# Performance work log

Hardware: AMD Instinct MI355X
Metric: run time of the kernel (lower is better)

The kernel has to match this reference:

```python
import jax, jax.numpy as jnp
import numpy as np

B, LQ, S, D, H = 8, 1024, 256, 1024, 16
HD = D // H
LN_EPS = 1e-5


def layer_norm(x, g, b):
    m = jnp.mean(x, axis=-1, keepdims=True)
    v = jnp.mean((x - m) ** 2, axis=-1, keepdims=True)
    return (x - m) / jnp.sqrt(v + LN_EPS) * g + b


def setup_inputs() -> dict:
    key = jax.random.key(0)
    ks = jax.random.split(key, 12)
    sc = 0.02
    p = lambda k, shp: jax.random.normal(k, shp, dtype=jnp.float32) * sc
    return {
        "memory": jax.random.normal(ks[0], (B, LQ, D // 2), dtype=jnp.float32),
        "gaze_features": jax.random.normal(ks[1], (B, LQ, D // 2), dtype=jnp.float32),
        "text_features": jax.random.normal(ks[2], (B, S, D), dtype=jnp.float32),
        "w_in": p(ks[3], (3 * D, D)),  # packed q,k,v in_proj (torch MHA layout)
        "b_in": jnp.zeros((3 * D,), jnp.float32),
        "w_o": p(ks[4], (D, D)),
        "b_o": jnp.zeros((D,), jnp.float32),
        "w1": p(ks[5], (D, D)),
        "b1": jnp.zeros((D,), jnp.float32),
        "w2": p(ks[6], (D, D)),
        "b2": jnp.zeros((D,), jnp.float32),
        "g1": jnp.ones((D,), jnp.float32),
        "be1": jnp.zeros((D,), jnp.float32),
        "g2": jnp.ones((D,), jnp.float32),
        "be2": jnp.zeros((D,), jnp.float32),
    }


def reference(memory, gaze_features, text_features, w_in, b_in, w_o, b_o,
              w1, b1, w2, b2, g1, be1, g2, be2):
    combined = jnp.concatenate([memory, gaze_features], axis=-1)  # [B, LQ, D]
    wq, wk, wv = w_in[:D], w_in[D:2 * D], w_in[2 * D:]
    bq, bk, bv = b_in[:D], b_in[D:2 * D], b_in[2 * D:]

    q = (combined @ wq.T + bq).reshape(B, LQ, H, HD)
    k = (text_features @ wk.T + bk).reshape(B, S, H, HD)
    v = (text_features @ wv.T + bv).reshape(B, S, H, HD)

    scores = jnp.einsum("bqhd,bkhd->bhqk", q, k) / jnp.sqrt(jnp.float32(HD))
    attn_w = jax.nn.softmax(scores, axis=-1)
    ctx = jnp.einsum("bhqk,bkhd->bqhd", attn_w, v).reshape(B, LQ, D)
    attn_output = ctx @ w_o.T + b_o  # [B, LQ, D]

    # dual FFN branches share linear1/linear2 (as in the source); dropout = eval identity
    ffn = jax.nn.relu(attn_output @ w1.T + b1) @ w2.T + b2
    refpoint_embed = layer_norm(ffn, g1, be1)
    tgt = layer_norm(ffn, g2, be2)

    # vectorized box decode (replaces the per-element Python loop)
    s = jax.nn.sigmoid(attn_output[..., :4])
    xc, yc, w, h = s[..., 0], s[..., 1], s[..., 2], s[..., 3]
    init_box_proposal = jnp.stack(
        [xc - w / 2, yc - h / 2, xc + w / 2, yc + h / 2], axis=-1)  # [B, LQ, 4]

    return refpoint_embed, tgt, init_box_proposal
```

## Files before the change

### kernel.cpp

```cpp
#include <hip/hip_runtime.h>


typedef unsigned short u16;
typedef unsigned int u32;
typedef __bf16 bf16x8 __attribute__((ext_vector_type(8)));
typedef float f32x4 __attribute__((ext_vector_type(4)));
typedef u16 u16x4 __attribute__((ext_vector_type(4)));

struct CvtArgs { const void* in[15]; };

__device__ __forceinline__ u16 f2bf(float f) {
  u32 u = __builtin_bit_cast(u32, f);
  u += 0x7fffu + ((u >> 16) & 1u);
  return (u16)(u >> 16);
}
__device__ __forceinline__ float bf2f(u16 h) {
  u32 u = ((u32)h) << 16;
  return __builtin_bit_cast(float, u);
}

struct WsPtrs {
  u16 *c_mem, *c_gaze, *c_text, *c_win, *c_bin, *c_wo, *c_bo, *c_w1, *c_b1,
      *c_w2, *c_b2, *c_g1, *c_be1, *c_g2, *c_be2;
  u16 *q, *k, *v, *ctx, *woT, *wf, *bfb, *h1, *ffnb;
};
__device__ __forceinline__ WsPtrs wsp(u16* C) {
  WsPtrs w;
  w.c_mem = C;                 w.c_gaze = C + 4194304;   w.c_text = C + 8388608;
  w.c_win = C + 10485760;      w.c_bin = C + 13631488;   w.c_wo = C + 13634560;
  w.c_bo = C + 14683136;       w.c_w1 = C + 14684160;    w.c_b1 = C + 15732736;
  w.c_w2 = C + 15733760;       w.c_b2 = C + 16782336;    w.c_g1 = C + 16783360;
  w.c_be1 = C + 16784384;      w.c_g2 = C + 16785408;    w.c_be2 = C + 16786432;
  u16* B2 = C + 16787488;
  w.q = B2;                    w.k = B2 + 8388608;       w.v = B2 + 10485760;
  w.ctx = B2 + 12582912;
  w.woT = B2 + 20971520;
  w.wf  = B2 + 22020096;
  w.bfb = B2 + 23068672;
  w.h1  = B2 + 29360128;
  w.ffnb = B2;
  return w;
}

__device__ __forceinline__ void cvt_chunk(bool f32in, u16* dst,
                                          const void* const* srcs, u32 c8) {
  const u32 cum[16] = {0u, 4194304u, 8388608u, 10485760u, 13631488u, 13634560u,
                       14683136u, 14684160u, 15732736u, 15733760u, 16782336u,
                       16783360u, 16784384u, 16785408u, 16786432u, 16787456u};
  u32 base = c8 * 8u;
  int idx = 0;
#pragma unroll
  for (int i = 1; i < 15; ++i) if (base >= cum[i]) idx = i;
  u32 off = base - cum[idx];
  if (f32in) {
    const float* s = (const float*)srcs[idx] + off;
    float4 a = ((const float4*)s)[0];
    float4 b = ((const float4*)s)[1];
    u16 t[8] = {f2bf(a.x), f2bf(a.y), f2bf(a.z), f2bf(a.w),
                f2bf(b.x), f2bf(b.y), f2bf(b.z), f2bf(b.w)};
    *(uint4*)(dst + base) = *(const uint4*)t;
  } else {
    *(uint4*)(dst + base) = *(const uint4*)((const u16*)srcs[idx] + off);
  }
}

__global__ __launch_bounds__(256) void cvt_tr(CvtArgs a, u16* ws) {
  __shared__ u16 tile[128 * 136];
  const bool f32in = (((const u32*)a.in[11])[0] == 0x3F800000u);
  const int bid = blockIdx.x, tid = threadIdx.x;
  if (bid < 64) {
    WsPtrs w = wsp(ws);
    int tr = bid >> 3, tc = bid & 7;
#pragma unroll
    for (int p = 0; p < 8; ++p) {
      int t = p * 16 + (tid >> 4);
      int j8 = (tid & 15) * 8;
      u16 tmp[8];
      if (f32in) {
        const float* s = (const float*)a.in[5] + (size_t)(tr * 128 + t) * 1024 + tc * 128 + j8;
        float4 x = ((const float4*)s)[0], y = ((const float4*)s)[1];
        tmp[0]=f2bf(x.x); tmp[1]=f2bf(x.y); tmp[2]=f2bf(x.z); tmp[3]=f2bf(x.w);
        tmp[4]=f2bf(y.x); tmp[5]=f2bf(y.y); tmp[6]=f2bf(y.z); tmp[7]=f2bf(y.w);
      } else {
        *(uint4*)tmp = *(const uint4*)((const u16*)a.in[5] + (size_t)(tr * 128 + t) * 1024 + tc * 128 + j8);
      }
      *(uint4*)&tile[t * 136 + j8] = *(const uint4*)tmp;
    }
    __syncthreads();
#pragma unroll
    for (int p = 0; p < 8; ++p) {
      int j = p * 16 + (tid >> 4);
      int t8 = (tid & 15) * 8;
      u16 tmp[8];
#pragma unroll
      for (int i = 0; i < 8; ++i) tmp[i] = tile[(t8 + i) * 136 + j];
      *(uint4*)(w.woT + (size_t)(tc * 128 + j) * 1024 + tr * 128 + t8) = *(const uint4*)tmp;
    }
  } else {
    u32 c8 = (u32)(bid - 64) * 256u + tid;
    if (c8 < 2098432u) cvt_chunk(f32in, ws, a.in, c8);
  }
}

template <int TN>
__device__ __forceinline__ void gemm_core(
    u16* sA, u16* sB,
    const u16* A0, const u16* A1, int Ksplit, int lda0, int lda1,
    const u16* W, const u16* bias, void* out, int N, int K,
    int mode, int lg, int m0, int n0)
{
  constexpr int JN = TN >> 5;
  constexpr int BCPT = TN >> 5;
  const int tid = threadIdx.x;
  const int wave = tid >> 6, lane = tid & 63;
  const int quad = lane >> 4, l16 = lane & 15;
  const int wm = wave >> 1, wn = wave & 1;

  f32x4 acc[4][JN];
#pragma unroll
  for (int i = 0; i < 4; ++i)
#pragma unroll
    for (int j = 0; j < JN; ++j) acc[i][j] = (f32x4){0.f, 0.f, 0.f, 0.f};

  for (int k0 = 0; k0 < K; k0 += 64) {
#pragma unroll
    for (int qi = 0; qi < 4; ++qi) {
      int p = (wave * 4 + qi) * 64 + lane;
      int row = p >> 3;
      int c = (p & 7) ^ (row & 7);
      int gk = k0 + (c << 3);
      const u16* srcA = (gk < Ksplit) ? (A0 + (size_t)(m0 + row) * lda0 + gk)
                                      : (A1 + (size_t)(m0 + row) * lda1 + (gk - Ksplit));
      __builtin_amdgcn_global_load_lds(
          (const __attribute__((address_space(1))) void*)srcA,
          (__attribute__((address_space(3))) void*)&sA[(size_t)(wave * 4 + qi) * 512],
          16, 0, 0);
    }
#pragma unroll
    for (int qi = 0; qi < BCPT; ++qi) {
      int p = (wave * BCPT + qi) * 64 + lane;
      int row = p >> 3;
      int c = (p & 7) ^ (row & 7);
      int gk = k0 + (c << 3);
      const u16* srcB = W + (size_t)(n0 + row) * K + gk;
      __builtin_amdgcn_global_load_lds(
          (const __attribute__((address_space(1))) void*)srcB,
          (__attribute__((address_space(3))) void*)&sB[(size_t)(wave * BCPT + qi) * 512],
          16, 0, 0);
    }
    __syncthreads();
#pragma unroll
    for (int ks = 0; ks < 2; ++ks) {
      const int ch = (ks << 2) + quad;
      bf16x8 af[4], bw[JN];
#pragma unroll
      for (int i = 0; i < 4; ++i) {
        int row = wm * 64 + i * 16 + l16;
        af[i] = *(const bf16x8*)&sA[(row << 6) + ((ch ^ (row & 7)) << 3)];
      }
#pragma unroll
      for (int j = 0; j < JN; ++j) {
        int row = wn * (TN >> 1) + j * 16 + l16;
        bw[j] = *(const bf16x8*)&sB[(row << 6) + ((ch ^ (row & 7)) << 3)];
      }
#pragma unroll
      for (int i = 0; i < 4; ++i)
#pragma unroll
        for (int j = 0; j < JN; ++j)
          acc[i][j] = __builtin_amdgcn_mfma_f32_16x16x32_bf16(af[i], bw[j], acc[i][j], 0, 0, 0);
    }
    __syncthreads();
  }

#pragma unroll
  for (int i = 0; i < 4; ++i) {
#pragma unroll
    for (int j = 0; j < JN; ++j) {
      int n = n0 + wn * (TN >> 1) + j * 16 + l16;
      float bv = bias ? bf2f(bias[n]) : 0.f;
#pragma unroll
      for (int rr = 0; rr < 4; ++rr) {
        int m = m0 + wm * 64 + i * 16 + quad * 4 + rr;
        float val = acc[i][j][rr] + bv;
        if (mode == 1) val = fmaxf(val, 0.f);
        if (mode <= 1) {
          ((u16*)out)[(size_t)m * N + n] = f2bf(val);
        } else if (mode == 3) {
          int b = m >> lg, l = m & ((1 << lg) - 1);
          int h = n >> 6, d = n & 63;
          ((u16*)out)[((size_t)((b * 16 + h)) << (lg + 6)) + (l << 6) + d] = f2bf(val);
        } else {
          int b = m >> lg, s = m & ((1 << lg) - 1);
          int h = n >> 6, d = n & 63;
          ((u16*)out)[((size_t)(((b * 16 + h) << 6) + d) << lg) + s] = f2bf(val);
        }
      }
    }
  }
}

__device__ __forceinline__ int xswz(int u, int n8) {
  return (u & 7) * n8 + (u >> 3);
}

__global__ __launch_bounds__(256, 4) void qkvwf(u16* ws) {
  __shared__ __align__(16) u16 lds[16384];
  WsPtrs w = wsp(ws);
  const int bid = blockIdx.x, tid = threadIdx.x;
  if (bid < 512) {
    int u = xswz(bid, 64);
    gemm_core<128>(lds, lds + 8192, w.c_mem, w.c_gaze, 512, 512, 512,
                   w.c_win, w.c_bin, w.q, 1024, 1024, 3, 10,
                   (u >> 3) * 128, (u & 7) * 128);
  } else if (bid < 640) {
    int u = xswz(bid - 512, 16);
    gemm_core<128>(lds, lds + 8192, w.c_text, w.c_text, 1024, 1024, 1024,
                   w.c_win + 1048576, w.c_bin + 1024, w.k, 1024, 1024, 3, 8,
                   (u >> 3) * 128, (u & 7) * 128);
  } else if (bid < 768) {
    int u = xswz(bid - 640, 16);
    gemm_core<128>(lds, lds + 8192, w.c_text, w.c_text, 1024, 1024, 1024,
                   w.c_win + 2097152, w.c_bin + 2048, w.v, 1024, 1024, 4, 8,
                   (u >> 3) * 128, (u & 7) * 128);
  } else if (bid < 832) {
    int u = xswz(bid - 768, 8);
    gemm_core<128>(lds, lds + 8192, w.c_w1, w.c_w1, 1024, 1024, 1024,
                   w.woT, nullptr, w.wf, 1024, 1024, 0, 0,
                   (u >> 3) * 128, (u & 7) * 128);
  } else {
    int i = (bid - 832) * 256 + tid;
    const u16* w1row = w.c_w1 + (size_t)i * 1024;
    float acc = bf2f(w.c_b1[i]);
    for (int kk = 0; kk < 1024; kk += 8) {
      bf16x8 wv = *(const bf16x8*)(w1row + kk);
      bf16x8 bv = *(const bf16x8*)(w.c_bo + kk);
#pragma unroll
      for (int j = 0; j < 8; ++j) acc += (float)wv[j] * (float)bv[j];
    }
    w.bfb[i] = f2bf(acc);
  }
}

__global__ __launch_bounds__(256) void attn_kernel(u16* ws) {
  __shared__ u16 sV[64 * 256];
  __shared__ u16 sKP[256 * 64];
  WsPtrs w = wsp(ws);
  const int tid = threadIdx.x;
  const int wave = tid >> 6, lane = tid & 63;
  const int quad = lane >> 4, l16 = lane & 15;
  const int su = xswz(blockIdx.x, 256);
  const int qb = su & 15, bh = su >> 4;

  {
    int rr = tid >> 3, c8 = (tid & 7) << 3;
    const u16* kb = w.k + (size_t)bh * 16384;
#pragma unroll
    for (int p = 0; p < 8; ++p) {
      int row = p * 32 + rr;
      uint4 val = *(const uint4*)(kb + row * 64 + c8);
      *(uint4*)&sKP[(row << 6) + ((((c8 >> 3) ^ (row & 7))) << 3)] = val;
    }
    int r2 = tid >> 5, c8b = (tid & 31) << 3;
    const u16* vb = w.v + (size_t)bh * 16384;
#pragma unroll
    for (int p = 0; p < 8; ++p) {
      int row = p * 8 + r2;
      uint4 val = *(const uint4*)(vb + (row << 8) + c8b);
      *(uint4*)&sV[(row << 8) + ((((c8b >> 3) ^ (row & 7))) << 3)] = val;
    }
  }
  bf16x8 aq[2];
  {
    const u16* qrow = w.q + ((size_t)bh * 1024 + qb * 64 + wave * 16 + l16) * 64 + quad * 8;
    aq[0] = *(const bf16x8*)(qrow);
    aq[1] = *(const bf16x8*)(qrow + 32);
  }
  __syncthreads();

  f32x4 sc[16];
#pragma unroll
  for (int nt = 0; nt < 16; ++nt) sc[nt] = (f32x4){0.f, 0.f, 0.f, 0.f};
  __builtin_amdgcn_s_setprio(1);
#pragma unroll
  for (int ks = 0; ks < 2; ++ks) {
    const int ch = (ks << 2) + quad;
#pragma unroll
    for (int nt = 0; nt < 16; ++nt) {
      int row = nt * 16 + l16;
      bf16x8 bk = *(const bf16x8*)&sKP[(row << 6) + ((ch ^ (row & 7)) << 3)];
      sc[nt] = __builtin_amdgcn_mfma_f32_16x16x32_bf16(aq[ks], bk, sc[nt], 0, 0, 0);
    }
  }
  __builtin_amdgcn_s_setprio(0);
#pragma unroll
  for (int rr = 0; rr < 4; ++rr) {
    float mx = -1e30f;
#pragma unroll
    for (int nt = 0; nt < 16; ++nt) mx = fmaxf(mx, sc[nt][rr]);
    for (int off = 1; off < 16; off <<= 1) mx = fmaxf(mx, __shfl_xor(mx, off, 64));
    float sum = 0.f;
#pragma unroll
    for (int nt = 0; nt < 16; ++nt) {
      float p = __expf((sc[nt][rr] - mx) * 0.125f);
      sc[nt][rr] = p; sum += p;
    }
    for (int off = 1; off < 16; off <<= 1) sum += __shfl_xor(sum, off, 64);
    float inv = 1.f / sum;
#pragma unroll
    for (int nt = 0; nt < 16; ++nt) sc[nt][rr] *= inv;
  }
  __syncthreads();
#pragma unroll
  for (int nt = 0; nt < 16; ++nt)
#pragma unroll
    for (int rr = 0; rr < 4; ++rr) {
      int row = wave * 16 + quad * 4 + rr;
      int col = nt * 16 + l16;
      sKP[(row << 8) + (((col >> 3) ^ (row & 7)) << 3) + (col & 7)] = f2bf(sc[nt][rr]);
    }
  __syncthreads();

  f32x4 o[4];
#pragma unroll
  for (int j = 0; j < 4; ++j) o[j] = (f32x4){0.f, 0.f, 0.f, 0.f};
  __builtin_amdgcn_s_setprio(1);
#pragma unroll
  for (int ks = 0; ks < 8; ++ks) {
    const int ch = (ks << 2) + quad;
    int prow = wave * 16 + l16;
    bf16x8 ap = *(const bf16x8*)&sKP[(prow << 8) + ((ch ^ (prow & 7)) << 3)];
#pragma unroll
    for (int j = 0; j < 4; ++j) {
      int vrow = j * 16 + l16;
      bf16x8 bv = *(const bf16x8*)&sV[(vrow << 8) + ((ch ^ (vrow & 7)) << 3)];
      o[j] = __builtin_amdgcn_mfma_f32_16x16x32_bf16(ap, bv, o[j], 0, 0, 0);
    }
  }
  __builtin_amdgcn_s_setprio(0);
  const int b = bh >> 4, h = bh & 15;
#pragma unroll
  for (int j = 0; j < 4; ++j)
#pragma unroll
    for (int rr = 0; rr < 4; ++rr) {
      int m = qb * 64 + wave * 16 + quad * 4 + rr;
      int d = h * 64 + j * 16 + l16;
      w.ctx[((size_t)b * 1024 + m) * 1024 + d] = f2bf(o[j][rr]);
    }
}

__global__ __launch_bounds__(256, 4) void h1box(u16* ws, void* out, const void* g1orig) {
  __shared__ __align__(16) u16 lds[12288];
  WsPtrs w = wsp(ws);
  const int u = blockIdx.x, tid = threadIdx.x;
  {
    const bool f32out = (((const u32*)g1orig)[0] == 0x3F800000u);
    int m = u * 8 + (tid >> 5);
    int l32 = tid & 31;
    int k0 = l32 * 32;
    const u16* crow = w.ctx + (size_t)m * 1024 + k0;
    float a0 = 0.f, a1 = 0.f, a2 = 0.f, a3 = 0.f;
#pragma unroll
    for (int kk = 0; kk < 32; kk += 8) {
      bf16x8 cv = *(const bf16x8*)(crow + kk);
      bf16x8 w0 = *(const bf16x8*)(w.c_wo + k0 + kk);
      bf16x8 w1v = *(const bf16x8*)(w.c_wo + 1024 + k0 + kk);
      bf16x8 w2v = *(const bf16x8*)(w.c_wo + 2048 + k0 + kk);
      bf16x8 w3v = *(const bf16x8*)(w.c_wo + 3072 + k0 + kk);
#pragma unroll
      for (int j = 0; j < 8; ++j) {
        float c = (float)cv[j];
        a0 += c * (float)w0[j]; a1 += c * (float)w1v[j];
        a2 += c * (float)w2v[j]; a3 += c * (float)w3v[j];
      }
    }
    for (int off = 1; off < 32; off <<= 1) {
      a0 += __shfl_xor(a0, off, 64); a1 += __shfl_xor(a1, off, 64);
      a2 += __shfl_xor(a2, off, 64); a3 += __shfl_xor(a3, off, 64);
    }
    if (l32 == 0) {
      a0 += bf2f(w.c_bo[0]); a1 += bf2f(w.c_bo[1]);
      a2 += bf2f(w.c_bo[2]); a3 += bf2f(w.c_bo[3]);
      float s0 = 1.f / (1.f + __expf(-a0)), s1 = 1.f / (1.f + __expf(-a1));
      float s2 = 1.f / (1.f + __expf(-a2)), s3 = 1.f / (1.f + __expf(-a3));
      float o0 = s0 - s2 * 0.5f, o1 = s1 - s3 * 0.5f;
      float o2 = s0 + s2 * 0.5f, o3 = s1 + s3 * 0.5f;
      if (f32out) {
        float* fo = (float*)out + 16777216;
        *(float4*)(fo + (size_t)m * 4) = make_float4(o0, o1, o2, o3);
      } else {
        u16* bo = (u16*)out + 16777216;
        u16x4 o; o[0] = f2bf(o0); o[1] = f2bf(o1); o[2] = f2bf(o2); o[3] = f2bf(o3);
        *(u16x4*)(bo + (size_t)m * 4) = o;
      }
    }
  }
  int us = xswz(u, 128);
  gemm_core<64>(lds, lds + 8192, w.ctx, w.ctx, 1024, 1024, 1024,
                w.wf, w.bfb, w.h1, 1024, 1024, 1, 0,
                (us >> 4) * 128, (us & 15) * 64);
}

__global__ __launch_bounds__(256, 4) void w2gemm(u16* ws) {
  __shared__ __align__(16) u16 lds[12288];
  WsPtrs w = wsp(ws);
  int us = xswz((int)blockIdx.x, 128);
  gemm_core<64>(lds, lds + 8192, w.h1, w.h1, 1024, 1024, 1024,
                w.c_w2, w.c_b2, w.ffnb, 1024, 1024, 0, 0,
                (us >> 4) * 128, (us & 15) * 64);
}

__global__ __launch_bounds__(256) void ln_kernel(u16* ws, void* outv, const void* g1orig) {
  WsPtrs w = wsp(ws);
  const bool f32out = (((const u32*)g1orig)[0] == 0x3F800000u);
  const int row = blockIdx.x, tid = threadIdx.x;
  int c = tid * 4;
  u16x4 xr = *(const u16x4*)(w.ffnb + (size_t)row * 1024 + c);
  float x[4] = {bf2f(xr[0]), bf2f(xr[1]), bf2f(xr[2]), bf2f(xr[3])};
  float s = x[0] + x[1] + x[2] + x[3];
  float s2 = x[0]*x[0] + x[1]*x[1] + x[2]*x[2] + x[3]*x[3];
  for (int m = 32; m >= 1; m >>= 1) { s += __shfl_xor(s, m, 64); s2 += __shfl_xor(s2, m, 64); }
  __shared__ float red[8];
  int wv = tid >> 6;
  if ((tid & 63) == 0) { red[wv] = s; red[4 + wv] = s2; }
  __syncthreads();
  s = red[0] + red[1] + red[2] + red[3];
  s2 = red[4] + red[5] + red[6] + red[7];
  float mean = s * (1.f / 1024.f);
  float var = s2 * (1.f / 1024.f) - mean * mean;
  float inv = rsqrtf(var + 1e-5f);
  float y[4] = {(x[0] - mean) * inv, (x[1] - mean) * inv, (x[2] - mean) * inv, (x[3] - mean) * inv};
  float v1[4], v2[4];
#pragma unroll
  for (int i = 0; i < 4; ++i) {
    v1[i] = y[i] * bf2f(w.c_g1[c + i]) + bf2f(w.c_be1[c + i]);
    v2[i] = y[i] * bf2f(w.c_g2[c + i]) + bf2f(w.c_be2[c + i]);
  }
  if (f32out) {
    float* fo = (float*)outv;
    *(float4*)(fo + (size_t)row * 1024 + c) = make_float4(v1[0], v1[1], v1[2], v1[3]);
    *(float4*)(fo + 8388608 + (size_t)row * 1024 + c) = make_float4(v2[0], v2[1], v2[2], v2[3]);
  } else {
    u16* out = (u16*)outv;
    u16x4 o1, o2;
#pragma unroll
    for (int i = 0; i < 4; ++i) { o1[i] = f2bf(v1[i]); o2[i] = f2bf(v2[i]); }
    *(u16x4*)(out + (size_t)row * 1024 + c) = o1;
    *(u16x4*)(out + 8388608 + (size_t)row * 1024 + c) = o2;
  }
}

extern "C" void kernel_launch(void* const* d_in, const int* in_sizes, int n_in,
                              void* d_out, int out_size, void* d_ws, size_t ws_size,
                              hipStream_t stream) {
  CvtArgs ca;
  for (int i = 0; i < 15; ++i) ca.in[i] = d_in[i];
  u16* ws = (u16*)d_ws;
  dim3 blk(256);
  cvt_tr<<<dim3(8261), blk, 0, stream>>>(ca, ws);
  qkvwf<<<dim3(836), blk, 0, stream>>>(ws);
  attn_kernel<<<dim3(2048), blk, 0, stream>>>(ws);
  h1box<<<dim3(1024), blk, 0, stream>>>(ws, d_out, d_in[11]);
  w2gemm<<<dim3(1024), blk, 0, stream>>>(ws);
  ln_kernel<<<dim3(8192), blk, 0, stream>>>(ws, d_out, d_in[11]);
}
```

Measured before the change: 290.4 us.

## Halve attention V smem, coarsen conversion and layernorm work per block

The attention kernel now stages V in two halves of 128 keys each. The second half is prefetched into registers during the first PV half, which halves the V shared-memory buffer and raises launch bounds to allow 3 blocks per CU. The conversion kernel processes four chunks per thread with a quarter of the blocks. The layernorm kernel handles two rows per block with 8-wide vector loads and stores. Together these aim to cut launch/block overhead and raise occupancy, at the cost of an extra sync and more registers in attention.

```diff
diff --git a/kernel.cpp b/kernel.cpp
--- a/kernel.cpp
+++ b/kernel.cpp
@@ -97,8 +97,12 @@
       *(uint4*)(w.woT + (size_t)(tc * 128 + j) * 1024 + tr * 128 + t8) = *(const uint4*)tmp;
     }
   } else {
-    u32 c8 = (u32)(bid - 64) * 256u + tid;
-    if (c8 < 2098432u) cvt_chunk(f32in, ws, a.in, c8);
+    u32 b = (u32)(bid - 64) * 1024u + tid;
+#pragma unroll
+    for (int k = 0; k < 4; ++k) {
+      u32 c8 = b + (u32)k * 256u;
+      if (c8 < 2098432u) cvt_chunk(f32in, ws, a.in, c8);
+    }
   }
 }
 
@@ -241,8 +245,8 @@
   }
 }
 
-__global__ __launch_bounds__(256) void attn_kernel(u16* ws) {
-  __shared__ u16 sV[64 * 256];
+__global__ __launch_bounds__(256, 3) void attn_kernel(u16* ws) {
+  __shared__ u16 sV[64 * 128];
   __shared__ u16 sKP[256 * 64];
   WsPtrs w = wsp(ws);
   const int tid = threadIdx.x;
@@ -250,24 +254,25 @@
   const int quad = lane >> 4, l16 = lane & 15;
   const int su = xswz(blockIdx.x, 256);
   const int qb = su & 15, bh = su >> 4;
+  const u16* kb = w.k + (size_t)bh * 16384;
+  const u16* vb = w.v + (size_t)bh * 16384;
 
   {
     int rr = tid >> 3, c8 = (tid & 7) << 3;
-    const u16* kb = w.k + (size_t)bh * 16384;
 #pragma unroll
     for (int p = 0; p < 8; ++p) {
       int row = p * 32 + rr;
       uint4 val = *(const uint4*)(kb + row * 64 + c8);
       *(uint4*)&sKP[(row << 6) + ((((c8 >> 3) ^ (row & 7))) << 3)] = val;
     }
-    int r2 = tid >> 5, c8b = (tid & 31) << 3;
-    const u16* vb = w.v + (size_t)bh * 16384;
-#pragma unroll
-    for (int p = 0; p < 8; ++p) {
-      int row = p * 8 + r2;
-      uint4 val = *(const uint4*)(vb + (row << 8) + c8b);
-      *(uint4*)&sV[(row << 8) + ((((c8b >> 3) ^ (row & 7))) << 3)] = val;
-    }
+  }
+  const int vr = tid >> 4;
+  const int vc8 = (tid & 15) << 3;
+#pragma unroll
+  for (int p = 0; p < 4; ++p) {
+    int row = p * 16 + vr;
+    uint4 val = *(const uint4*)(vb + (row << 8) + vc8);
+    *(uint4*)&sV[(row << 7) + ((((vc8 >> 3) ^ (row & 7))) << 3)] = val;
   }
   bf16x8 aq[2];
   {
@@ -320,19 +325,48 @@
     }
   __syncthreads();
 
+  uint4 v1r[4];
+#pragma unroll
+  for (int p = 0; p < 4; ++p) {
+    int row = p * 16 + vr;
+    v1r[p] = *(const uint4*)(vb + (row << 8) + 128 + vc8);
+  }
+
   f32x4 o[4];
 #pragma unroll
   for (int j = 0; j < 4; ++j) o[j] = (f32x4){0.f, 0.f, 0.f, 0.f};
   __builtin_amdgcn_s_setprio(1);
 #pragma unroll
-  for (int ks = 0; ks < 8; ++ks) {
+  for (int ks = 0; ks < 4; ++ks) {
     const int ch = (ks << 2) + quad;
     int prow = wave * 16 + l16;
     bf16x8 ap = *(const bf16x8*)&sKP[(prow << 8) + ((ch ^ (prow & 7)) << 3)];
 #pragma unroll
     for (int j = 0; j < 4; ++j) {
       int vrow = j * 16 + l16;
-      bf16x8 bv = *(const bf16x8*)&sV[(vrow << 8) + ((ch ^ (vrow & 7)) << 3)];
+      bf16x8 bv = *(const bf16x8*)&sV[(vrow << 7) + ((ch ^ (vrow & 7)) << 3)];
+      o[j] = __builtin_amdgcn_mfma_f32_16x16x32_bf16(ap, bv, o[j], 0, 0, 0);
+    }
+  }
+  __builtin_amdgcn_s_setprio(0);
+  __syncthreads();
+#pragma unroll
+  for (int p = 0; p < 4; ++p) {
+    int row = p * 16 + vr;
+    *(uint4*)&sV[(row << 7) + ((((vc8 >> 3) ^ (row & 7))) << 3)] = v1r[p];
+  }
+  __syncthreads();
+  __builtin_amdgcn_s_setprio(1);
+#pragma unroll
+  for (int ks = 4; ks < 8; ++ks) {
+    const int ch = (ks << 2) + quad;
+    const int chl = ch & 15;
+    int prow = wave * 16 + l16;
+    bf16x8 ap = *(const bf16x8*)&sKP[(prow << 8) + ((ch ^ (prow & 7)) << 3)];
+#pragma unroll
+    for (int j = 0; j < 4; ++j) {
+      int vrow = j * 16 + l16;
+      bf16x8 bv = *(const bf16x8*)&sV[(vrow << 7) + ((chl ^ (vrow & 7)) << 3)];
       o[j] = __builtin_amdgcn_mfma_f32_16x16x32_bf16(ap, bv, o[j], 0, 0, 0);
     }
   }
@@ -412,40 +446,55 @@
 __global__ __launch_bounds__(256) void ln_kernel(u16* ws, void* outv, const void* g1orig) {
   WsPtrs w = wsp(ws);
   const bool f32out = (((const u32*)g1orig)[0] == 0x3F800000u);
-  const int row = blockIdx.x, tid = threadIdx.x;
-  int c = tid * 4;
-  u16x4 xr = *(const u16x4*)(w.ffnb + (size_t)row * 1024 + c);
-  float x[4] = {bf2f(xr[0]), bf2f(xr[1]), bf2f(xr[2]), bf2f(xr[3])};
-  float s = x[0] + x[1] + x[2] + x[3];
-  float s2 = x[0]*x[0] + x[1]*x[1] + x[2]*x[2] + x[3]*x[3];
+  const int tid = threadIdx.x;
+  const int rhalf = tid >> 7;
+  const int row = blockIdx.x * 2 + rhalf;
+  const int c = (tid & 127) * 8;
+  uint4 xr = *(const uint4*)(w.ffnb + (size_t)row * 1024 + c);
+  const u16* xp = (const u16*)&xr;
+  float x[8];
+  float s = 0.f, s2 = 0.f;
+#pragma unroll
+  for (int i = 0; i < 8; ++i) {
+    x[i] = bf2f(xp[i]);
+    s += x[i]; s2 += x[i] * x[i];
+  }
   for (int m = 32; m >= 1; m >>= 1) { s += __shfl_xor(s, m, 64); s2 += __shfl_xor(s2, m, 64); }
   __shared__ float red[8];
   int wv = tid >> 6;
   if ((tid & 63) == 0) { red[wv] = s; red[4 + wv] = s2; }
   __syncthreads();
-  s = red[0] + red[1] + red[2] + red[3];
-  s2 = red[4] + red[5] + red[6] + red[7];
+  s = red[rhalf * 2] + red[rhalf * 2 + 1];
+  s2 = red[4 + rhalf * 2] + red[4 + rhalf * 2 + 1];
   float mean = s * (1.f / 1024.f);
   float var = s2 * (1.f / 1024.f) - mean * mean;
   float inv = rsqrtf(var + 1e-5f);
-  float y[4] = {(x[0] - mean) * inv, (x[1] - mean) * inv, (x[2] - mean) * inv, (x[3] - mean) * inv};
-  float v1[4], v2[4];
-#pragma unroll
-  for (int i = 0; i < 4; ++i) {
-    v1[i] = y[i] * bf2f(w.c_g1[c + i]) + bf2f(w.c_be1[c + i]);
-    v2[i] = y[i] * bf2f(w.c_g2[c + i]) + bf2f(w.c_be2[c + i]);
+  uint4 g1r = *(const uint4*)(w.c_g1 + c);
+  uint4 b1r = *(const uint4*)(w.c_be1 + c);
+  uint4 g2r = *(const uint4*)(w.c_g2 + c);
+  uint4 b2r = *(const uint4*)(w.c_be2 + c);
+  const u16* g1p = (const u16*)&g1r; const u16* b1p = (const u16*)&b1r;
+  const u16* g2p = (const u16*)&g2r; const u16* b2p = (const u16*)&b2r;
+  float v1[8], v2[8];
+#pragma unroll
+  for (int i = 0; i < 8; ++i) {
+    float y = (x[i] - mean) * inv;
+    v1[i] = y * bf2f(g1p[i]) + bf2f(b1p[i]);
+    v2[i] = y * bf2f(g2p[i]) + bf2f(b2p[i]);
   }
   if (f32out) {
     float* fo = (float*)outv;
     *(float4*)(fo + (size_t)row * 1024 + c) = make_float4(v1[0], v1[1], v1[2], v1[3]);
+    *(float4*)(fo + (size_t)row * 1024 + c + 4) = make_float4(v1[4], v1[5], v1[6], v1[7]);
     *(float4*)(fo + 8388608 + (size_t)row * 1024 + c) = make_float4(v2[0], v2[1], v2[2], v2[3]);
+    *(float4*)(fo + 8388608 + (size_t)row * 1024 + c + 4) = make_float4(v2[4], v2[5], v2[6], v2[7]);
   } else {
     u16* out = (u16*)outv;
-    u16x4 o1, o2;
-#pragma unroll
-    for (int i = 0; i < 4; ++i) { o1[i] = f2bf(v1[i]); o2[i] = f2bf(v2[i]); }
-    *(u16x4*)(out + (size_t)row * 1024 + c) = o1;
-    *(u16x4*)(out + 8388608 + (size_t)row * 1024 + c) = o2;
+    u16 o1[8], o2[8];
+#pragma unroll
+    for (int i = 0; i < 8; ++i) { o1[i] = f2bf(v1[i]); o2[i] = f2bf(v2[i]); }
+    *(uint4*)(out + (size_t)row * 1024 + c) = *(const uint4*)o1;
+    *(uint4*)(out + 8388608 + (size_t)row * 1024 + c) = *(const uint4*)o2;
   }
 }
 
@@ -456,10 +505,10 @@
   for (int i = 0; i < 15; ++i) ca.in[i] = d_in[i];
   u16* ws = (u16*)d_ws;
   dim3 blk(256);
-  cvt_tr<<<dim3(8261), blk, 0, stream>>>(ca, ws);
+  cvt_tr<<<dim3(2114), blk, 0, stream>>>(ca, ws);
   qkvwf<<<dim3(836), blk, 0, stream>>>(ws);
   attn_kernel<<<dim3(2048), blk, 0, stream>>>(ws);
   h1box<<<dim3(1024), blk, 0, stream>>>(ws, d_out, d_in[11]);
   w2gemm<<<dim3(1024), blk, 0, stream>>>(ws);
-  ln_kernel<<<dim3(8192), blk, 0, stream>>>(ws, d_out, d_in[11]);
-}
+  ln_kernel<<<dim3(4096), blk, 0, stream>>>(ws, d_out, d_in[11]);
+}
```

New measurement: 312.5 us. 7.6% more time.
